# Kernel optimization log

Hardware: AMD Instinct MI355X
Metric: run time of the kernel (lower is better)

Reference implementation:

```python
import jax, jax.numpy as jnp
import numpy as np

N_NODES = 100000
N_EDGES = 1600000
IN_CH, HID_CH, OUT_CH = 128, 64, 40


def setup_inputs() -> dict:
    key = jax.random.key(0)
    k_x, k_e, k_w1, k_w2 = jax.random.split(key, 4)
    x = jax.random.normal(k_x, (N_NODES, IN_CH), dtype=jnp.float32)
    edge_index = jax.random.randint(k_e, (2, N_EDGES), 0, N_NODES, dtype=jnp.int64)
    # Glorot-ish scaled weights, zero bias (matches GCNConv init convention)
    W1 = jax.random.normal(k_w1, (IN_CH, HID_CH), dtype=jnp.float32) / np.sqrt(IN_CH)
    b1 = jnp.zeros((HID_CH,), dtype=jnp.float32)
    W2 = jax.random.normal(k_w2, (HID_CH, OUT_CH), dtype=jnp.float32) / np.sqrt(HID_CH)
    b2 = jnp.zeros((OUT_CH,), dtype=jnp.float32)
    return {"x": x, "edge_index": edge_index, "W1": W1, "b1": b1, "W2": W2, "b2": b2}


def _gcn_conv(x, edge_index, W, b, n):
    """GCNConv with normalize=True: linear transform, add self-loops,
    symmetric D^-1/2 A D^-1/2 aggregation (source_to_target flow), bias."""
    h = x @ W  # [n, out]
    loops = jnp.arange(n, dtype=edge_index.dtype)
    row = jnp.concatenate([edge_index[0], loops])  # sources
    col = jnp.concatenate([edge_index[1], loops])  # targets
    deg = jax.ops.segment_sum(jnp.ones_like(col, dtype=h.dtype), col, num_segments=n)
    dinv = jnp.where(deg > 0, jax.lax.rsqrt(deg), jnp.zeros_like(deg))
    w = dinv[row] * dinv[col]  # [E+n] per-edge norm
    out = jax.ops.segment_sum(h[row] * w[:, None], col, num_segments=n)  # scatter-add to targets
    return out + b


def reference(x, edge_index, W1, b1, W2, b2):
    # eval mode: F.dropout(p=0.8, training=False) is identity
    n = x.shape[0]
    h = jax.nn.relu(_gcn_conv(x, edge_index, W1, b1, n))
    return _gcn_conv(h, edge_index, W2, b2, n)  # [N, OUT_CH] logits
```

## Files before the change

kernel.cpp:

```cpp
#include <hip/hip_runtime.h>

#define N_NODES 100000
#define N_EDGES 1600000
#define IN_CH   128
#define HID_CH  64
#define OUT_CH  40
#define NBKT    196
#define EPB     4096
#define CAP     9216

using bf16x8 = __attribute__((ext_vector_type(8))) short;
using f32x4  = __attribute__((ext_vector_type(4))) float;

__device__ __forceinline__ float bf2f(unsigned short u) {
    union { unsigned int i; float f; } c; c.i = ((unsigned int)u) << 16; return c.f;
}
__device__ __forceinline__ unsigned short f2bf(float f) {
    union { float f; unsigned int i; } c; c.f = f;
    unsigned int r = c.i + 0x7FFFu + ((c.i >> 16) & 1u);
    return (unsigned short)(r >> 16);
}
__device__ __forceinline__ float4 bf2f4(ushort4 u) {
    return make_float4(bf2f(u.x), bf2f(u.y), bf2f(u.z), bf2f(u.w));
}

__global__ void k_bin(const int* __restrict__ ei, int* __restrict__ gcur,
                      int* __restrict__ ebuf) {
    __shared__ int hist[NBKT];
    __shared__ int lcur[NBKT];
    int tid = threadIdx.x;
    int base = blockIdx.x * EPB;
    int nloc = N_EDGES - base;
    if (nloc > EPB) nloc = EPB;
    int n4 = nloc >> 2;
    const int4* S4 = (const int4*)(ei + base);
    const int4* D4 = (const int4*)(ei + N_EDGES + base);

    if (tid < NBKT) { hist[tid] = 0; }
    __syncthreads();
    for (int i = tid; i < n4; i += 256) {
        int4 d = D4[i];
        atomicAdd(&hist[d.x >> 9], 1);
        atomicAdd(&hist[d.y >> 9], 1);
        atomicAdd(&hist[d.z >> 9], 1);
        atomicAdd(&hist[d.w >> 9], 1);
    }
    __syncthreads();
    if (tid < NBKT) {
        int h = hist[tid];
        lcur[tid] = h ? (tid * CAP + atomicAdd(&gcur[tid], h)) : 0;
    }
    __syncthreads();
    for (int i = tid; i < n4; i += 256) {
        int4 s = S4[i];
        int4 d = D4[i];
        int p;
        p = atomicAdd(&lcur[d.x >> 9], 1); ebuf[p] = s.x | ((d.x & 511) << 17);
        p = atomicAdd(&lcur[d.y >> 9], 1); ebuf[p] = s.y | ((d.y & 511) << 17);
        p = atomicAdd(&lcur[d.z >> 9], 1); ebuf[p] = s.z | ((d.z & 511) << 17);
        p = atomicAdd(&lcur[d.w >> 9], 1); ebuf[p] = s.w | ((d.w & 511) << 17);
    }
}

__global__ void k_node(const int* __restrict__ gcur, const int* __restrict__ ebuf,
                       int* __restrict__ row_start, int* __restrict__ row_end,
                       int* __restrict__ csr_src, float* __restrict__ dinv) {
    __shared__ int cnt[512];
    __shared__ int s[512];
    int tid = threadIdx.x;
    int b = blockIdx.x;
    int node0 = b << 9;
    int lo = b * CAP;
    int hi = lo + gcur[b];
    int n = hi - lo, n4 = n >> 2;
    const int4* E4 = (const int4*)(ebuf + lo);

    cnt[tid] = 0;
    __syncthreads();
    for (int i = tid; i < n4; i += 512) {
        int4 w = E4[i];
        atomicAdd(&cnt[(unsigned)w.x >> 17], 1);
        atomicAdd(&cnt[(unsigned)w.y >> 17], 1);
        atomicAdd(&cnt[(unsigned)w.z >> 17], 1);
        atomicAdd(&cnt[(unsigned)w.w >> 17], 1);
    }
    for (int e = lo + (n4 << 2) + tid; e < hi; e += 512)
        atomicAdd(&cnt[(unsigned)ebuf[e] >> 17], 1);
    __syncthreads();
    int c = cnt[tid];
    s[tid] = c;
    __syncthreads();
#pragma unroll
    for (int off = 1; off < 512; off <<= 1) {
        int tv = (tid >= off) ? s[tid - off] : 0;
        __syncthreads();
        s[tid] += tv;
        __syncthreads();
    }
    int node = node0 + tid;
    if (node < N_NODES) {
        row_start[node] = lo + s[tid] - c;
        row_end[node]   = lo + s[tid];
        dinv[node] = rsqrtf(1.0f + (float)c);
    }
    __syncthreads();
    cnt[tid] = lo + s[tid] - c;
    __syncthreads();
    for (int i = tid; i < n4; i += 512) {
        int4 w = E4[i];
        int p;
        p = atomicAdd(&cnt[(unsigned)w.x >> 17], 1); csr_src[p] = w.x & 0x1FFFF;
        p = atomicAdd(&cnt[(unsigned)w.y >> 17], 1); csr_src[p] = w.y & 0x1FFFF;
        p = atomicAdd(&cnt[(unsigned)w.z >> 17], 1); csr_src[p] = w.z & 0x1FFFF;
        p = atomicAdd(&cnt[(unsigned)w.w >> 17], 1); csr_src[p] = w.w & 0x1FFFF;
    }
    for (int e = lo + (n4 << 2) + tid; e < hi; e += 512) {
        int w = ebuf[e];
        int p = atomicAdd(&cnt[(unsigned)w >> 17], 1);
        csr_src[p] = w & 0x1FFFF;
    }
}

__global__ __launch_bounds__(256, 4)
void k_gemm1(const float* __restrict__ x, const float* __restrict__ W1,
             const float* __restrict__ dinv, unsigned short* __restrict__ h1s) {
    __shared__ unsigned short Al[64 * 136];
    __shared__ unsigned short Bl[64 * 136];
    __shared__ float dl[64];
    int tid = threadIdx.x;
    long long node0 = (long long)blockIdx.x * 64;

    const float4* X = (const float4*)x;
    for (int i = tid; i < 64 * 32; i += 256) {
        int r = i >> 5, c4 = i & 31;
        long long gr = node0 + r;
        if (gr >= N_NODES) gr = N_NODES - 1;
        float4 v = X[gr * 32 + c4];
        *(ushort4*)&Al[r * 136 + c4 * 4] =
            make_ushort4(f2bf(v.x), f2bf(v.y), f2bf(v.z), f2bf(v.w));
    }
    for (int i = tid; i < 128 * 64; i += 256) {
        int k = i >> 6, nn = i & 63;
        Bl[nn * 136 + k] = f2bf(W1[i]);
    }
    if (tid < 64) {
        long long gr = node0 + tid;
        dl[tid] = dinv[gr < N_NODES ? gr : N_NODES - 1];
    }
    __syncthreads();

    int lane = tid & 63, wave = tid >> 6;
    int quad = lane >> 4, l16 = lane & 15;
    int arow = wave * 16 + l16;
    f32x4 ac0 = {0,0,0,0}, ac1 = {0,0,0,0}, ac2 = {0,0,0,0}, ac3 = {0,0,0,0};

#pragma unroll
    for (int ks = 0; ks < 4; ++ks) {
        int ko = ks * 32 + quad * 8;
        bf16x8 a  = *(const bf16x8*)&Al[arow * 136 + ko];
        bf16x8 b0 = *(const bf16x8*)&Bl[( 0 + l16) * 136 + ko];
        bf16x8 b1 = *(const bf16x8*)&Bl[(16 + l16) * 136 + ko];
        bf16x8 b2 = *(const bf16x8*)&Bl[(32 + l16) * 136 + ko];
        bf16x8 b3 = *(const bf16x8*)&Bl[(48 + l16) * 136 + ko];
        ac0 = __builtin_amdgcn_mfma_f32_16x16x32_bf16(a, b0, ac0, 0, 0, 0);
        ac1 = __builtin_amdgcn_mfma_f32_16x16x32_bf16(a, b1, ac1, 0, 0, 0);
        ac2 = __builtin_amdgcn_mfma_f32_16x16x32_bf16(a, b2, ac2, 0, 0, 0);
        ac3 = __builtin_amdgcn_mfma_f32_16x16x32_bf16(a, b3, ac3, 0, 0, 0);
    }

#pragma unroll
    for (int r = 0; r < 4; ++r) {
        int rl = wave * 16 + quad * 4 + r;
        long long grow = node0 + rl;
        if (grow < N_NODES) {
            float dd = dl[rl];
            h1s[grow * 64 +  0 + l16] = f2bf(ac0[r] * dd);
            h1s[grow * 64 + 16 + l16] = f2bf(ac1[r] * dd);
            h1s[grow * 64 + 32 + l16] = f2bf(ac2[r] * dd);
            h1s[grow * 64 + 48 + l16] = f2bf(ac3[r] * dd);
        }
    }
}

__global__ __launch_bounds__(256, 4)
void k_agg1g2(const int* __restrict__ row_start, const int* __restrict__ row_end,
              const int* __restrict__ csr_src,
              const unsigned short* __restrict__ h1s, const float* __restrict__ dinv,
              const float* __restrict__ b1, const float* __restrict__ W2,
              unsigned short* __restrict__ h2s) {
    __shared__ unsigned short Al[64 * 72];
    __shared__ unsigned short Bl[48 * 72];
    __shared__ float dl[64];
    int tid = threadIdx.x;
    long long node0 = (long long)blockIdx.x * 64;

    for (int i = tid; i < 48 * 64; i += 256) {
        int nn = i >> 6, k = i & 63;
        Bl[nn * 72 + k] = f2bf(nn < OUT_CH ? W2[k * OUT_CH + nn] : 0.0f);
    }
    if (tid < 64) {
        long long gr = node0 + tid;
        dl[tid] = dinv[gr < N_NODES ? gr : N_NODES - 1];
    }
    __syncthreads();

    int cg = tid & 15;
    int nsub = tid >> 4;
    float4 bb = ((const float4*)b1)[cg];
    const ushort4* H = (const ushort4*)h1s;

#pragma unroll
    for (int r4 = 0; r4 < 4; ++r4) {
        int nl = r4 * 16 + nsub;
        long long node = node0 + nl;
        ushort4 res = make_ushort4(0, 0, 0, 0);
        if (node < N_NODES) {
            int e = row_start[node];
            int f = row_end[node];
            float4 acc = bf2f4(H[node * 16 + cg]);
            float4 acc2 = {0.f, 0.f, 0.f, 0.f};
            while (f - e >= 8) {
                int s0 = csr_src[e];
                int s1 = csr_src[e + 1];
                int s2 = csr_src[e + 2];
                int s3 = csr_src[e + 3];
                int t0 = csr_src[f - 4];
                int t1 = csr_src[f - 3];
                int t2 = csr_src[f - 2];
                int t3 = csr_src[f - 1];
                float4 v0 = bf2f4(H[(long long)s0 * 16 + cg]);
                float4 v1 = bf2f4(H[(long long)s1 * 16 + cg]);
                float4 v2 = bf2f4(H[(long long)s2 * 16 + cg]);
                float4 v3 = bf2f4(H[(long long)s3 * 16 + cg]);
                float4 u0 = bf2f4(H[(long long)t0 * 16 + cg]);
                float4 u1 = bf2f4(H[(long long)t1 * 16 + cg]);
                float4 u2 = bf2f4(H[(long long)t2 * 16 + cg]);
                float4 u3 = bf2f4(H[(long long)t3 * 16 + cg]);
                acc.x  += (v0.x + v1.x) + (v2.x + v3.x);
                acc.y  += (v0.y + v1.y) + (v2.y + v3.y);
                acc.z  += (v0.z + v1.z) + (v2.z + v3.z);
                acc.w  += (v0.w + v1.w) + (v2.w + v3.w);
                acc2.x += (u0.x + u1.x) + (u2.x + u3.x);
                acc2.y += (u0.y + u1.y) + (u2.y + u3.y);
                acc2.z += (u0.z + u1.z) + (u2.z + u3.z);
                acc2.w += (u0.w + u1.w) + (u2.w + u3.w);
                e += 4; f -= 4;
            }
            for (; e < f; ++e) {
                float4 v = bf2f4(H[(long long)csr_src[e] * 16 + cg]);
                acc.x += v.x; acc.y += v.y; acc.z += v.z; acc.w += v.w;
            }
            acc.x += acc2.x; acc.y += acc2.y; acc.z += acc2.z; acc.w += acc2.w;
            float dd = dl[nl];
            res = make_ushort4(f2bf(fmaxf(acc.x * dd + bb.x, 0.f)),
                               f2bf(fmaxf(acc.y * dd + bb.y, 0.f)),
                               f2bf(fmaxf(acc.z * dd + bb.z, 0.f)),
                               f2bf(fmaxf(acc.w * dd + bb.w, 0.f)));
        }
        *(ushort4*)&Al[nl * 72 + cg * 4] = res;
    }
    __syncthreads();

    int lane = tid & 63, wave = tid >> 6;
    int quad = lane >> 4, l16 = lane & 15;
    int arow = wave * 16 + l16;
    f32x4 ac0 = {0,0,0,0}, ac1 = {0,0,0,0}, ac2 = {0,0,0,0};

#pragma unroll
    for (int ks = 0; ks < 2; ++ks) {
        int ko = ks * 32 + quad * 8;
        bf16x8 a  = *(const bf16x8*)&Al[arow * 72 + ko];
        bf16x8 b0 = *(const bf16x8*)&Bl[( 0 + l16) * 72 + ko];
        bf16x8 b1v = *(const bf16x8*)&Bl[(16 + l16) * 72 + ko];
        bf16x8 b2 = *(const bf16x8*)&Bl[(32 + l16) * 72 + ko];
        ac0 = __builtin_amdgcn_mfma_f32_16x16x32_bf16(a, b0, ac0, 0, 0, 0);
        ac1 = __builtin_amdgcn_mfma_f32_16x16x32_bf16(a, b1v, ac1, 0, 0, 0);
        ac2 = __builtin_amdgcn_mfma_f32_16x16x32_bf16(a, b2, ac2, 0, 0, 0);
    }

#pragma unroll
    for (int r = 0; r < 4; ++r) {
        int rl = wave * 16 + quad * 4 + r;
        long long grow = node0 + rl;
        if (grow < N_NODES) {
            float dd = dl[rl];
            h2s[grow * 40 +  0 + l16] = f2bf(ac0[r] * dd);
            h2s[grow * 40 + 16 + l16] = f2bf(ac1[r] * dd);
            if (l16 < 8) h2s[grow * 40 + 32 + l16] = f2bf(ac2[r] * dd);
        }
    }
}

__global__ void k_agg2(const int* __restrict__ row_start, const int* __restrict__ row_end,
                       const int* __restrict__ csr_src,
                       const unsigned short* __restrict__ h2s, const float* __restrict__ dinv,
                       const float* __restrict__ b2, float* __restrict__ out) {
    int idx = blockIdx.x * blockDim.x + threadIdx.x;
    int node = idx >> 4;
    int cg = idx & 15;
    if (node >= N_NODES || cg >= 10) return;
    int e = row_start[node];
    int f = row_end[node];
    const ushort4* H = (const ushort4*)h2s;
    float4 acc = bf2f4(H[(long long)node * 10 + cg]);
    float4 acc2 = {0.f, 0.f, 0.f, 0.f};
    while (f - e >= 8) {
        int s0 = csr_src[e];
        int s1 = csr_src[e + 1];
        int s2 = csr_src[e + 2];
        int s3 = csr_src[e + 3];
        int t0 = csr_src[f - 4];
        int t1 = csr_src[f - 3];
        int t2 = csr_src[f - 2];
        int t3 = csr_src[f - 1];
        float4 v0 = bf2f4(H[(long long)s0 * 10 + cg]);
        float4 v1 = bf2f4(H[(long long)s1 * 10 + cg]);
        float4 v2 = bf2f4(H[(long long)s2 * 10 + cg]);
        float4 v3 = bf2f4(H[(long long)s3 * 10 + cg]);
        float4 u0 = bf2f4(H[(long long)t0 * 10 + cg]);
        float4 u1 = bf2f4(H[(long long)t1 * 10 + cg]);
        float4 u2 = bf2f4(H[(long long)t2 * 10 + cg]);
        float4 u3 = bf2f4(H[(long long)t3 * 10 + cg]);
        acc.x  += (v0.x + v1.x) + (v2.x + v3.x);
        acc.y  += (v0.y + v1.y) + (v2.y + v3.y);
        acc.z  += (v0.z + v1.z) + (v2.z + v3.z);
        acc.w  += (v0.w + v1.w) + (v2.w + v3.w);
        acc2.x += (u0.x + u1.x) + (u2.x + u3.x);
        acc2.y += (u0.y + u1.y) + (u2.y + u3.y);
        acc2.z += (u0.z + u1.z) + (u2.z + u3.z);
        acc2.w += (u0.w + u1.w) + (u2.w + u3.w);
        e += 4; f -= 4;
    }
    for (; e < f; ++e) {
        float4 v = bf2f4(H[(long long)csr_src[e] * 10 + cg]);
        acc.x += v.x; acc.y += v.y; acc.z += v.z; acc.w += v.w;
    }
    acc.x += acc2.x; acc.y += acc2.y; acc.z += acc2.z; acc.w += acc2.w;
    float dd = dinv[node];
    float4 b = ((const float4*)b2)[cg];
    acc.x = acc.x * dd + b.x;
    acc.y = acc.y * dd + b.y;
    acc.z = acc.z * dd + b.z;
    acc.w = acc.w * dd + b.w;
    ((float4*)out)[(long long)node * 10 + cg] = acc;
}

extern "C" void kernel_launch(void* const* d_in, const int* in_sizes, int n_in,
                              void* d_out, int out_size, void* d_ws, size_t ws_size,
                              hipStream_t stream) {
    const float* x  = (const float*)d_in[0];
    const int*   ei = (const int*)d_in[1];
    const float* W1 = (const float*)d_in[2];
    const float* b1 = (const float*)d_in[3];
    const float* W2 = (const float*)d_in[4];
    const float* b2 = (const float*)d_in[5];
    float* out = (float*)d_out;

    unsigned short* hbuf  = (unsigned short*)d_ws;
    unsigned short* h2buf = hbuf + 64LL * N_NODES;
    int* ebuf      = (int*)(h2buf + 64LL * N_NODES);
    int* csr_src   = ebuf + NBKT * CAP;
    int* row_start = csr_src + NBKT * CAP;
    int* row_end   = row_start + N_NODES;
    int* gcur      = row_end + N_NODES;
    float* dinv    = (float*)(gcur + 256);

    const int B = 256;
    const int g16 = (N_NODES * 16 + B - 1) / B;
    const int gRows = (N_NODES + 63) / 64;

    hipMemsetAsync((void*)gcur, 0, NBKT * sizeof(int), stream);
    k_bin<<<(N_EDGES + EPB - 1) / EPB, B, 0, stream>>>(ei, gcur, ebuf);
    k_node<<<NBKT, 512, 0, stream>>>(gcur, ebuf, row_start, row_end, csr_src, dinv);

    k_gemm1<<<gRows, B, 0, stream>>>(x, W1, dinv, hbuf);
    k_agg1g2<<<gRows, B, 0, stream>>>(row_start, row_end, csr_src, hbuf, dinv,
                                      b1, W2, h2buf);
    k_agg2<<<g16, B, 0, stream>>>(row_start, row_end, csr_src, h2buf, dinv, b2, out);
}
```

Baseline: 223.5 us.

## Build CSR with global atomics and cooperative shuffle-based neighbor gathers

Replaces the two-pass bucket binning CSR build with a degree count using global atomics, a per-block scan, and a placement pass using global atomic cursors. This drops the intermediate edge buffer and the shared-memory histogram passes but adds heavy contention on global atomics. Both aggregation kernels now have the 16 lanes of each node load 16 neighbor indices together and broadcast them with shuffles, keeping four accumulators. The aim is to coalesce index loads and expose more memory parallelism, at the cost of wasted lanes when a node has few neighbors.

```diff
diff --git a/kernel.cpp b/kernel.cpp
--- a/kernel.cpp
+++ b/kernel.cpp
@@ -6,8 +6,8 @@
 #define HID_CH  64
 #define OUT_CH  40
 #define NBKT    196
-#define EPB     4096
 #define CAP     9216
+#define NE4     (N_EDGES / 4)
 
 using bf16x8 = __attribute__((ext_vector_type(8))) short;
 using f32x4  = __attribute__((ext_vector_type(4))) float;
@@ -24,71 +24,25 @@
     return make_float4(bf2f(u.x), bf2f(u.y), bf2f(u.z), bf2f(u.w));
 }
 
-__global__ void k_bin(const int* __restrict__ ei, int* __restrict__ gcur,
-                      int* __restrict__ ebuf) {
-    __shared__ int hist[NBKT];
-    __shared__ int lcur[NBKT];
-    int tid = threadIdx.x;
-    int base = blockIdx.x * EPB;
-    int nloc = N_EDGES - base;
-    if (nloc > EPB) nloc = EPB;
-    int n4 = nloc >> 2;
-    const int4* S4 = (const int4*)(ei + base);
-    const int4* D4 = (const int4*)(ei + N_EDGES + base);
-
-    if (tid < NBKT) { hist[tid] = 0; }
-    __syncthreads();
-    for (int i = tid; i < n4; i += 256) {
-        int4 d = D4[i];
-        atomicAdd(&hist[d.x >> 9], 1);
-        atomicAdd(&hist[d.y >> 9], 1);
-        atomicAdd(&hist[d.z >> 9], 1);
-        atomicAdd(&hist[d.w >> 9], 1);
-    }
-    __syncthreads();
-    if (tid < NBKT) {
-        int h = hist[tid];
-        lcur[tid] = h ? (tid * CAP + atomicAdd(&gcur[tid], h)) : 0;
-    }
-    __syncthreads();
-    for (int i = tid; i < n4; i += 256) {
-        int4 s = S4[i];
-        int4 d = D4[i];
-        int p;
-        p = atomicAdd(&lcur[d.x >> 9], 1); ebuf[p] = s.x | ((d.x & 511) << 17);
-        p = atomicAdd(&lcur[d.y >> 9], 1); ebuf[p] = s.y | ((d.y & 511) << 17);
-        p = atomicAdd(&lcur[d.z >> 9], 1); ebuf[p] = s.z | ((d.z & 511) << 17);
-        p = atomicAdd(&lcur[d.w >> 9], 1); ebuf[p] = s.w | ((d.w & 511) << 17);
-    }
-}
-
-__global__ void k_node(const int* __restrict__ gcur, const int* __restrict__ ebuf,
-                       int* __restrict__ row_start, int* __restrict__ row_end,
-                       int* __restrict__ csr_src, float* __restrict__ dinv) {
-    __shared__ int cnt[512];
+__global__ void k_deg(const int* __restrict__ ei, int* __restrict__ dgr) {
+    int i = blockIdx.x * blockDim.x + threadIdx.x;
+    if (i >= NE4) return;
+    const int4* D4 = (const int4*)(ei + N_EDGES);
+    int4 d = D4[i];
+    atomicAdd(dgr + d.x, 1);
+    atomicAdd(dgr + d.y, 1);
+    atomicAdd(dgr + d.z, 1);
+    atomicAdd(dgr + d.w, 1);
+}
+
+__global__ void k_scan(const int* __restrict__ dgr, int* __restrict__ row_start,
+                       int* __restrict__ row_end, int* __restrict__ cursor,
+                       float* __restrict__ dinv) {
     __shared__ int s[512];
-    int tid = threadIdx.x;
-    int b = blockIdx.x;
-    int node0 = b << 9;
-    int lo = b * CAP;
-    int hi = lo + gcur[b];
-    int n = hi - lo, n4 = n >> 2;
-    const int4* E4 = (const int4*)(ebuf + lo);
-
-    cnt[tid] = 0;
-    __syncthreads();
-    for (int i = tid; i < n4; i += 512) {
-        int4 w = E4[i];
-        atomicAdd(&cnt[(unsigned)w.x >> 17], 1);
-        atomicAdd(&cnt[(unsigned)w.y >> 17], 1);
-        atomicAdd(&cnt[(unsigned)w.z >> 17], 1);
-        atomicAdd(&cnt[(unsigned)w.w >> 17], 1);
-    }
-    for (int e = lo + (n4 << 2) + tid; e < hi; e += 512)
-        atomicAdd(&cnt[(unsigned)ebuf[e] >> 17], 1);
-    __syncthreads();
-    int c = cnt[tid];
-    s[tid] = c;
+    int tid = threadIdx.x, b = blockIdx.x;
+    int node = (b << 9) + tid;
+    int d = (node < N_NODES) ? dgr[node] : 0;
+    s[tid] = d;
     __syncthreads();
 #pragma unroll
     for (int off = 1; off < 512; off <<= 1) {
@@ -97,28 +51,28 @@
         s[tid] += tv;
         __syncthreads();
     }
-    int node = node0 + tid;
     if (node < N_NODES) {
-        row_start[node] = lo + s[tid] - c;
-        row_end[node]   = lo + s[tid];
-        dinv[node] = rsqrtf(1.0f + (float)c);
-    }
-    __syncthreads();
-    cnt[tid] = lo + s[tid] - c;
-    __syncthreads();
-    for (int i = tid; i < n4; i += 512) {
-        int4 w = E4[i];
-        int p;
-        p = atomicAdd(&cnt[(unsigned)w.x >> 17], 1); csr_src[p] = w.x & 0x1FFFF;
-        p = atomicAdd(&cnt[(unsigned)w.y >> 17], 1); csr_src[p] = w.y & 0x1FFFF;
-        p = atomicAdd(&cnt[(unsigned)w.z >> 17], 1); csr_src[p] = w.z & 0x1FFFF;
-        p = atomicAdd(&cnt[(unsigned)w.w >> 17], 1); csr_src[p] = w.w & 0x1FFFF;
-    }
-    for (int e = lo + (n4 << 2) + tid; e < hi; e += 512) {
-        int w = ebuf[e];
-        int p = atomicAdd(&cnt[(unsigned)w >> 17], 1);
-        csr_src[p] = w & 0x1FFFF;
-    }
+        int start = b * CAP + s[tid] - d;
+        row_start[node] = start;
+        row_end[node]   = start + d;
+        cursor[node]    = start;
+        dinv[node]      = rsqrtf(1.0f + (float)d);
+    }
+}
+
+__global__ void k_place(const int* __restrict__ ei, int* __restrict__ cursor,
+                        int* __restrict__ csr_src) {
+    int i = blockIdx.x * blockDim.x + threadIdx.x;
+    if (i >= NE4) return;
+    const int4* S4 = (const int4*)ei;
+    const int4* D4 = (const int4*)(ei + N_EDGES);
+    int4 s = S4[i];
+    int4 d = D4[i];
+    int p;
+    p = atomicAdd(cursor + d.x, 1); csr_src[p] = s.x;
+    p = atomicAdd(cursor + d.y, 1); csr_src[p] = s.y;
+    p = atomicAdd(cursor + d.z, 1); csr_src[p] = s.z;
+    p = atomicAdd(cursor + d.w, 1); csr_src[p] = s.w;
 }
 
 __global__ __launch_bounds__(256, 4)
@@ -216,46 +170,33 @@
         ushort4 res = make_ushort4(0, 0, 0, 0);
         if (node < N_NODES) {
             int e = row_start[node];
-            int f = row_end[node];
-            float4 acc = bf2f4(H[node * 16 + cg]);
-            float4 acc2 = {0.f, 0.f, 0.f, 0.f};
-            while (f - e >= 8) {
-                int s0 = csr_src[e];
-                int s1 = csr_src[e + 1];
-                int s2 = csr_src[e + 2];
-                int s3 = csr_src[e + 3];
-                int t0 = csr_src[f - 4];
-                int t1 = csr_src[f - 3];
-                int t2 = csr_src[f - 2];
-                int t3 = csr_src[f - 1];
-                float4 v0 = bf2f4(H[(long long)s0 * 16 + cg]);
-                float4 v1 = bf2f4(H[(long long)s1 * 16 + cg]);
-                float4 v2 = bf2f4(H[(long long)s2 * 16 + cg]);
-                float4 v3 = bf2f4(H[(long long)s3 * 16 + cg]);
-                float4 u0 = bf2f4(H[(long long)t0 * 16 + cg]);
-                float4 u1 = bf2f4(H[(long long)t1 * 16 + cg]);
-                float4 u2 = bf2f4(H[(long long)t2 * 16 + cg]);
-                float4 u3 = bf2f4(H[(long long)t3 * 16 + cg]);
-                acc.x  += (v0.x + v1.x) + (v2.x + v3.x);
-                acc.y  += (v0.y + v1.y) + (v2.y + v3.y);
-                acc.z  += (v0.z + v1.z) + (v2.z + v3.z);
-                acc.w  += (v0.w + v1.w) + (v2.w + v3.w);
-                acc2.x += (u0.x + u1.x) + (u2.x + u3.x);
-                acc2.y += (u0.y + u1.y) + (u2.y + u3.y);
-                acc2.z += (u0.z + u1.z) + (u2.z + u3.z);
-                acc2.w += (u0.w + u1.w) + (u2.w + u3.w);
-                e += 4; f -= 4;
+            int nd = row_end[node] - e;
+            float4 a0 = bf2f4(H[node * 16 + cg]);
+            float4 a1 = {0.f,0.f,0.f,0.f}, a2 = {0.f,0.f,0.f,0.f}, a3 = {0.f,0.f,0.f,0.f};
+            while (nd > 0) {
+                int kk = cg < nd ? cg : nd - 1;
+                int idxr = csr_src[e + kk];
+                int K = nd < 16 ? nd : 16;
+#define GSTEP(J, A) { int ss = __shfl(idxr, J, 16); \
+                      ushort4 rw = H[(long long)ss * 16 + cg]; \
+                      if (J < K) { float4 v = bf2f4(rw); \
+                        A.x += v.x; A.y += v.y; A.z += v.z; A.w += v.w; } }
+                GSTEP( 0, a0) GSTEP( 1, a1) GSTEP( 2, a2) GSTEP( 3, a3)
+                GSTEP( 4, a0) GSTEP( 5, a1) GSTEP( 6, a2) GSTEP( 7, a3)
+                GSTEP( 8, a0) GSTEP( 9, a1) GSTEP(10, a2) GSTEP(11, a3)
+                GSTEP(12, a0) GSTEP(13, a1) GSTEP(14, a2) GSTEP(15, a3)
+#undef GSTEP
+                e += 16; nd -= 16;
             }
-            for (; e < f; ++e) {
-                float4 v = bf2f4(H[(long long)csr_src[e] * 16 + cg]);
-                acc.x += v.x; acc.y += v.y; acc.z += v.z; acc.w += v.w;
-            }
-            acc.x += acc2.x; acc.y += acc2.y; acc.z += acc2.z; acc.w += acc2.w;
+            a0.x += a1.x + a2.x + a3.x;
+            a0.y += a1.y + a2.y + a3.y;
+            a0.z += a1.z + a2.z + a3.z;
+            a0.w += a1.w + a2.w + a3.w;
             float dd = dl[nl];
-            res = make_ushort4(f2bf(fmaxf(acc.x * dd + bb.x, 0.f)),
-                               f2bf(fmaxf(acc.y * dd + bb.y, 0.f)),
-                               f2bf(fmaxf(acc.z * dd + bb.z, 0.f)),
-                               f2bf(fmaxf(acc.w * dd + bb.w, 0.f)));
+            res = make_ushort4(f2bf(fmaxf(a0.x * dd + bb.x, 0.f)),
+                               f2bf(fmaxf(a0.y * dd + bb.y, 0.f)),
+                               f2bf(fmaxf(a0.z * dd + bb.z, 0.f)),
+                               f2bf(fmaxf(a0.w * dd + bb.w, 0.f)));
         }
         *(ushort4*)&Al[nl * 72 + cg * 4] = res;
     }
@@ -291,58 +232,49 @@
     }
 }
 
-__global__ void k_agg2(const int* __restrict__ row_start, const int* __restrict__ row_end,
-                       const int* __restrict__ csr_src,
-                       const unsigned short* __restrict__ h2s, const float* __restrict__ dinv,
-                       const float* __restrict__ b2, float* __restrict__ out) {
+__global__ __launch_bounds__(256, 4)
+void k_agg2(const int* __restrict__ row_start, const int* __restrict__ row_end,
+            const int* __restrict__ csr_src,
+            const unsigned short* __restrict__ h2s, const float* __restrict__ dinv,
+            const float* __restrict__ b2, float* __restrict__ out) {
     int idx = blockIdx.x * blockDim.x + threadIdx.x;
     int node = idx >> 4;
     int cg = idx & 15;
-    if (node >= N_NODES || cg >= 10) return;
+    if (node >= N_NODES) return;
     int e = row_start[node];
-    int f = row_end[node];
+    int nd = row_end[node] - e;
     const ushort4* H = (const ushort4*)h2s;
-    float4 acc = bf2f4(H[(long long)node * 10 + cg]);
-    float4 acc2 = {0.f, 0.f, 0.f, 0.f};
-    while (f - e >= 8) {
-        int s0 = csr_src[e];
-        int s1 = csr_src[e + 1];
-        int s2 = csr_src[e + 2];
-        int s3 = csr_src[e + 3];
-        int t0 = csr_src[f - 4];
-        int t1 = csr_src[f - 3];
-        int t2 = csr_src[f - 2];
-        int t3 = csr_src[f - 1];
-        float4 v0 = bf2f4(H[(long long)s0 * 10 + cg]);
-        float4 v1 = bf2f4(H[(long long)s1 * 10 + cg]);
-        float4 v2 = bf2f4(H[(long long)s2 * 10 + cg]);
-        float4 v3 = bf2f4(H[(long long)s3 * 10 + cg]);
-        float4 u0 = bf2f4(H[(long long)t0 * 10 + cg]);
-        float4 u1 = bf2f4(H[(long long)t1 * 10 + cg]);
-        float4 u2 = bf2f4(H[(long long)t2 * 10 + cg]);
-        float4 u3 = bf2f4(H[(long long)t3 * 10 + cg]);
-        acc.x  += (v0.x + v1.x) + (v2.x + v3.x);
-        acc.y  += (v0.y + v1.y) + (v2.y + v3.y);
-        acc.z  += (v0.z + v1.z) + (v2.z + v3.z);
-        acc.w  += (v0.w + v1.w) + (v2.w + v3.w);
-        acc2.x += (u0.x + u1.x) + (u2.x + u3.x);
-        acc2.y += (u0.y + u1.y) + (u2.y + u3.y);
-        acc2.z += (u0.z + u1.z) + (u2.z + u3.z);
-        acc2.w += (u0.w + u1.w) + (u2.w + u3.w);
-        e += 4; f -= 4;
-    }
-    for (; e < f; ++e) {
-        float4 v = bf2f4(H[(long long)csr_src[e] * 10 + cg]);
-        acc.x += v.x; acc.y += v.y; acc.z += v.z; acc.w += v.w;
-    }
-    acc.x += acc2.x; acc.y += acc2.y; acc.z += acc2.z; acc.w += acc2.w;
-    float dd = dinv[node];
-    float4 b = ((const float4*)b2)[cg];
-    acc.x = acc.x * dd + b.x;
-    acc.y = acc.y * dd + b.y;
-    acc.z = acc.z * dd + b.z;
-    acc.w = acc.w * dd + b.w;
-    ((float4*)out)[(long long)node * 10 + cg] = acc;
+    bool act = cg < 10;
+    float4 a0 = {0.f,0.f,0.f,0.f}, a1 = a0, a2 = a0, a3 = a0;
+    if (act) a0 = bf2f4(H[(long long)node * 10 + cg]);
+    while (nd > 0) {
+        int kk = cg < nd ? cg : nd - 1;
+        int idxr = csr_src[e + kk];
+        int K = nd < 16 ? nd : 16;
+#define GSTEP2(J, A) { int ss = __shfl(idxr, J, 16); \
+                       if (act && J < K) { \
+                         float4 v = bf2f4(H[(long long)ss * 10 + cg]); \
+                         A.x += v.x; A.y += v.y; A.z += v.z; A.w += v.w; } }
+        GSTEP2( 0, a0) GSTEP2( 1, a1) GSTEP2( 2, a2) GSTEP2( 3, a3)
+        GSTEP2( 4, a0) GSTEP2( 5, a1) GSTEP2( 6, a2) GSTEP2( 7, a3)
+        GSTEP2( 8, a0) GSTEP2( 9, a1) GSTEP2(10, a2) GSTEP2(11, a3)
+        GSTEP2(12, a0) GSTEP2(13, a1) GSTEP2(14, a2) GSTEP2(15, a3)
+#undef GSTEP2
+        e += 16; nd -= 16;
+    }
+    if (act) {
+        a0.x += a1.x + a2.x + a3.x;
+        a0.y += a1.y + a2.y + a3.y;
+        a0.z += a1.z + a2.z + a3.z;
+        a0.w += a1.w + a2.w + a3.w;
+        float dd = dinv[node];
+        float4 b = ((const float4*)b2)[cg];
+        a0.x = a0.x * dd + b.x;
+        a0.y = a0.y * dd + b.y;
+        a0.z = a0.z * dd + b.z;
+        a0.w = a0.w * dd + b.w;
+        ((float4*)out)[(long long)node * 10 + cg] = a0;
+    }
 }
 
 extern "C" void kernel_launch(void* const* d_in, const int* in_sizes, int n_in,
@@ -358,20 +290,22 @@
 
     unsigned short* hbuf  = (unsigned short*)d_ws;
     unsigned short* h2buf = hbuf + 64LL * N_NODES;
-    int* ebuf      = (int*)(h2buf + 64LL * N_NODES);
-    int* csr_src   = ebuf + NBKT * CAP;
+    int* csr_src   = (int*)(h2buf + 40LL * N_NODES);
     int* row_start = csr_src + NBKT * CAP;
     int* row_end   = row_start + N_NODES;
-    int* gcur      = row_end + N_NODES;
-    float* dinv    = (float*)(gcur + 256);
+    int* cursor    = row_end + N_NODES;
+    int* dgr       = cursor + N_NODES;
+    float* dinv    = (float*)(dgr + N_NODES);
 
     const int B = 256;
-    const int g16 = (N_NODES * 16 + B - 1) / B;
+    const int gE   = (NE4 + B - 1) / B;
+    const int g16  = (N_NODES * 16 + B - 1) / B;
     const int gRows = (N_NODES + 63) / 64;
 
-    hipMemsetAsync((void*)gcur, 0, NBKT * sizeof(int), stream);
-    k_bin<<<(N_EDGES + EPB - 1) / EPB, B, 0, stream>>>(ei, gcur, ebuf);
-    k_node<<<NBKT, 512, 0, stream>>>(gcur, ebuf, row_start, row_end, csr_src, dinv);
+    hipMemsetAsync((void*)dgr, 0, N_NODES * sizeof(int), stream);
+    k_deg<<<gE, B, 0, stream>>>(ei, dgr);
+    k_scan<<<NBKT, 512, 0, stream>>>(dgr, row_start, row_end, cursor, dinv);
+    k_place<<<gE, B, 0, stream>>>(ei, cursor, csr_src);
 
     k_gemm1<<<gRows, B, 0, stream>>>(x, W1, dinv, hbuf);
     k_agg1g2<<<gRows, B, 0, stream>>>(row_start, row_end, csr_src, hbuf, dinv,
```

Measured after the change: 391.2 us. 75.0% more time.

## Sort CSR neighbors by source window for gather locality; forward-only unroll

Applied to the files above, without the earlier changes.

The CSR build kernel now counts edges per (target node, source-window) pair, where each window covers 8192 source ids, and prefix-sums within each node. Each node's neighbor list therefore comes out grouped by source window, so the aggregation gathers hit nearby rows of H and should get better cache locality. The aggregation loops now read eight consecutive neighbor indices from the front instead of four from each end. The cost is a 17x larger shared-memory counter array in k_node, which lowers its occupancy and adds extra zeroing and a per-thread scan.

```diff
diff --git a/kernel.cpp b/kernel.cpp
--- a/kernel.cpp
+++ b/kernel.cpp
@@ -8,6 +8,8 @@
 #define NBKT    196
 #define EPB     4096
 #define CAP     9216
+#define NWIN    16
+#define WPITCH  17
 
 using bf16x8 = __attribute__((ext_vector_type(8))) short;
 using f32x4  = __attribute__((ext_vector_type(4))) float;
@@ -65,7 +67,7 @@
 __global__ void k_node(const int* __restrict__ gcur, const int* __restrict__ ebuf,
                        int* __restrict__ row_start, int* __restrict__ row_end,
                        int* __restrict__ csr_src, float* __restrict__ dinv) {
-    __shared__ int cnt[512];
+    __shared__ int cnt2[512 * WPITCH];
     __shared__ int s[512];
     int tid = threadIdx.x;
     int b = blockIdx.x;
@@ -75,19 +77,28 @@
     int n = hi - lo, n4 = n >> 2;
     const int4* E4 = (const int4*)(ebuf + lo);
 
-    cnt[tid] = 0;
+#define BIN_OF(w) (((unsigned)(w) >> 17) * WPITCH + (((w) & 0x1FFFF) >> 13))
+
+    for (int i = tid; i < 512 * WPITCH; i += 512) cnt2[i] = 0;
     __syncthreads();
     for (int i = tid; i < n4; i += 512) {
         int4 w = E4[i];
-        atomicAdd(&cnt[(unsigned)w.x >> 17], 1);
-        atomicAdd(&cnt[(unsigned)w.y >> 17], 1);
-        atomicAdd(&cnt[(unsigned)w.z >> 17], 1);
-        atomicAdd(&cnt[(unsigned)w.w >> 17], 1);
+        atomicAdd(&cnt2[BIN_OF(w.x)], 1);
+        atomicAdd(&cnt2[BIN_OF(w.y)], 1);
+        atomicAdd(&cnt2[BIN_OF(w.z)], 1);
+        atomicAdd(&cnt2[BIN_OF(w.w)], 1);
     }
     for (int e = lo + (n4 << 2) + tid; e < hi; e += 512)
-        atomicAdd(&cnt[(unsigned)ebuf[e] >> 17], 1);
-    __syncthreads();
-    int c = cnt[tid];
+        atomicAdd(&cnt2[BIN_OF(ebuf[e])], 1);
+    __syncthreads();
+
+    int tmp[NWIN];
+    int c = 0;
+#pragma unroll
+    for (int w = 0; w < NWIN; ++w) {
+        tmp[w] = c;
+        c += cnt2[tid * WPITCH + w];
+    }
     s[tid] = c;
     __syncthreads();
 #pragma unroll
@@ -97,28 +108,32 @@
         s[tid] += tv;
         __syncthreads();
     }
+    int nodestart = lo + s[tid] - c;
     int node = node0 + tid;
     if (node < N_NODES) {
-        row_start[node] = lo + s[tid] - c;
-        row_end[node]   = lo + s[tid];
+        row_start[node] = nodestart;
+        row_end[node]   = nodestart + c;
         dinv[node] = rsqrtf(1.0f + (float)c);
     }
-    __syncthreads();
-    cnt[tid] = lo + s[tid] - c;
-    __syncthreads();
+#pragma unroll
+    for (int w = 0; w < NWIN; ++w)
+        cnt2[tid * WPITCH + w] = nodestart + tmp[w];
+    __syncthreads();
+
     for (int i = tid; i < n4; i += 512) {
         int4 w = E4[i];
         int p;
-        p = atomicAdd(&cnt[(unsigned)w.x >> 17], 1); csr_src[p] = w.x & 0x1FFFF;
-        p = atomicAdd(&cnt[(unsigned)w.y >> 17], 1); csr_src[p] = w.y & 0x1FFFF;
-        p = atomicAdd(&cnt[(unsigned)w.z >> 17], 1); csr_src[p] = w.z & 0x1FFFF;
-        p = atomicAdd(&cnt[(unsigned)w.w >> 17], 1); csr_src[p] = w.w & 0x1FFFF;
+        p = atomicAdd(&cnt2[BIN_OF(w.x)], 1); csr_src[p] = w.x & 0x1FFFF;
+        p = atomicAdd(&cnt2[BIN_OF(w.y)], 1); csr_src[p] = w.y & 0x1FFFF;
+        p = atomicAdd(&cnt2[BIN_OF(w.z)], 1); csr_src[p] = w.z & 0x1FFFF;
+        p = atomicAdd(&cnt2[BIN_OF(w.w)], 1); csr_src[p] = w.w & 0x1FFFF;
     }
     for (int e = lo + (n4 << 2) + tid; e < hi; e += 512) {
         int w = ebuf[e];
-        int p = atomicAdd(&cnt[(unsigned)w >> 17], 1);
+        int p = atomicAdd(&cnt2[BIN_OF(w)], 1);
         csr_src[p] = w & 0x1FFFF;
     }
+#undef BIN_OF
 }
 
 __global__ __launch_bounds__(256, 4)
@@ -224,18 +239,18 @@
                 int s1 = csr_src[e + 1];
                 int s2 = csr_src[e + 2];
                 int s3 = csr_src[e + 3];
-                int t0 = csr_src[f - 4];
-                int t1 = csr_src[f - 3];
-                int t2 = csr_src[f - 2];
-                int t3 = csr_src[f - 1];
+                int s4 = csr_src[e + 4];
+                int s5 = csr_src[e + 5];
+                int s6 = csr_src[e + 6];
+                int s7 = csr_src[e + 7];
                 float4 v0 = bf2f4(H[(long long)s0 * 16 + cg]);
                 float4 v1 = bf2f4(H[(long long)s1 * 16 + cg]);
                 float4 v2 = bf2f4(H[(long long)s2 * 16 + cg]);
                 float4 v3 = bf2f4(H[(long long)s3 * 16 + cg]);
-                float4 u0 = bf2f4(H[(long long)t0 * 16 + cg]);
-                float4 u1 = bf2f4(H[(long long)t1 * 16 + cg]);
-                float4 u2 = bf2f4(H[(long long)t2 * 16 + cg]);
-                float4 u3 = bf2f4(H[(long long)t3 * 16 + cg]);
+                float4 u0 = bf2f4(H[(long long)s4 * 16 + cg]);
+                float4 u1 = bf2f4(H[(long long)s5 * 16 + cg]);
+                float4 u2 = bf2f4(H[(long long)s6 * 16 + cg]);
+                float4 u3 = bf2f4(H[(long long)s7 * 16 + cg]);
                 acc.x  += (v0.x + v1.x) + (v2.x + v3.x);
                 acc.y  += (v0.y + v1.y) + (v2.y + v3.y);
                 acc.z  += (v0.z + v1.z) + (v2.z + v3.z);
@@ -244,7 +259,7 @@
                 acc2.y += (u0.y + u1.y) + (u2.y + u3.y);
                 acc2.z += (u0.z + u1.z) + (u2.z + u3.z);
                 acc2.w += (u0.w + u1.w) + (u2.w + u3.w);
-                e += 4; f -= 4;
+                e += 8;
             }
             for (; e < f; ++e) {
                 float4 v = bf2f4(H[(long long)csr_src[e] * 16 + cg]);
@@ -309,18 +324,18 @@
         int s1 = csr_src[e + 1];
         int s2 = csr_src[e + 2];
         int s3 = csr_src[e + 3];
-        int t0 = csr_src[f - 4];
-        int t1 = csr_src[f - 3];
-        int t2 = csr_src[f - 2];
-        int t3 = csr_src[f - 1];
+        int s4 = csr_src[e + 4];
+        int s5 = csr_src[e + 5];
+        int s6 = csr_src[e + 6];
+        int s7 = csr_src[e + 7];
         float4 v0 = bf2f4(H[(long long)s0 * 10 + cg]);
         float4 v1 = bf2f4(H[(long long)s1 * 10 + cg]);
         float4 v2 = bf2f4(H[(long long)s2 * 10 + cg]);
         float4 v3 = bf2f4(H[(long long)s3 * 10 + cg]);
-        float4 u0 = bf2f4(H[(long long)t0 * 10 + cg]);
-        float4 u1 = bf2f4(H[(long long)t1 * 10 + cg]);
-        float4 u2 = bf2f4(H[(long long)t2 * 10 + cg]);
-        float4 u3 = bf2f4(H[(long long)t3 * 10 + cg]);
+        float4 u0 = bf2f4(H[(long long)s4 * 10 + cg]);
+        float4 u1 = bf2f4(H[(long long)s5 * 10 + cg]);
+        float4 u2 = bf2f4(H[(long long)s6 * 10 + cg]);
+        float4 u3 = bf2f4(H[(long long)s7 * 10 + cg]);
         acc.x  += (v0.x + v1.x) + (v2.x + v3.x);
         acc.y  += (v0.y + v1.y) + (v2.y + v3.y);
         acc.z  += (v0.z + v1.z) + (v2.z + v3.z);
@@ -329,7 +344,7 @@
         acc2.y += (u0.y + u1.y) + (u2.y + u3.y);
         acc2.z += (u0.z + u1.z) + (u2.z + u3.z);
         acc2.w += (u0.w + u1.w) + (u2.w + u3.w);
-        e += 4; f -= 4;
+        e += 8;
     }
     for (; e < f; ++e) {
         float4 v = bf2f4(H[(long long)csr_src[e] * 10 + cg]);
```

Measured after the change: 225.1 us. Within noise of the previous version (+0.7%).
